# Performance work log

Measured on AMD Instinct MI355X. Metric: run time of the kernel, lower is better.

## Reference

```python
import jax, jax.numpy as jnp
import numpy as np

N = 50000      # nodes
E = 800000     # edges
F = 128        # feat_dim
N_RBF = 20
CUTOFF = 5.0


def setup_inputs() -> dict:
    key = jax.random.key(0)
    ks = jax.random.split(key, 10)
    s_j = jax.random.normal(ks[0], (N, F), dtype=jnp.float32)
    v_j = jax.random.normal(ks[1], (N, F, 3), dtype=jnp.float32)
    r_ij = jax.random.normal(ks[2], (E, 3), dtype=jnp.float32)
    nbrs = jax.random.randint(ks[3], (E, 2), 0, N, dtype=jnp.int64)
    # inv_dense: Dense(F->F, swish) then Dense(F->2F)
    W1 = jax.random.normal(ks[4], (F, F), dtype=jnp.float32) / np.sqrt(F)
    b1 = jnp.zeros((F,), dtype=jnp.float32)
    W2 = jax.random.normal(ks[5], (F, 2 * F), dtype=jnp.float32) / np.sqrt(F)
    b2 = jnp.zeros((2 * F,), dtype=jnp.float32)
    # dist_embed: PainnRadialBasis(n_rbf) -> Dense(n_rbf -> 2F), cosine envelope
    Wd = jax.random.normal(ks[6], (N_RBF, 2 * F), dtype=jnp.float32) / np.sqrt(N_RBF)
    bd = jnp.zeros((2 * F,), dtype=jnp.float32)
    return {"s_j": s_j, "v_j": v_j, "r_ij": r_ij, "nbrs": nbrs,
            "W1": W1, "b1": b1, "W2": W2, "b2": b2, "Wd": Wd, "bd": bd}


def reference(s_j, v_j, r_ij, nbrs, W1, b1, W2, b2, Wd, bd):
    # preprocess_r
    dist = jnp.sqrt(jnp.sum(r_ij ** 2 + 1e-8, axis=-1))        # [E]
    unit = r_ij / dist[:, None]                                 # [E,3]

    # InvariantMessage: per-node MLP then gather sender features
    h = jax.nn.silu(s_j @ W1 + b1)                              # [N,F]
    phi_all = h @ W2 + b2                                       # [N,2F]
    phi = phi_all[nbrs[:, 1]]                                   # [E,2F]

    # DistanceEmbed: PaiNN radial basis sin(n*pi*d/cutoff)/d -> Dense -> cosine envelope
    n = jnp.arange(1, N_RBF + 1, dtype=dist.dtype)              # [n_rbf]
    rbf = jnp.sin(n[None, :] * jnp.pi * dist[:, None] / CUTOFF) / dist[:, None]  # [E,n_rbf]
    w_s = rbf @ Wd + bd                                         # [E,2F]
    env = jnp.where(dist < CUTOFF, 0.5 * (jnp.cos(jnp.pi * dist / CUTOFF) + 1.0), 0.0)
    w_s = w_s * env[:, None]

    inv_out = (phi * w_s).reshape(E, 2, F)                      # [E,2,F]
    equi_filter = inv_out[:, 0, :][:, :, None]                  # [E,F,1]
    inv_filter = inv_out[:, 1, :]                               # [E,F]

    delta_v_ij = equi_filter * unit[:, None, :]                 # [E,F,3]
    dest = nbrs[:, 0]
    delta_v_i = jax.ops.segment_sum(delta_v_ij, dest, num_segments=N)  # [N,F,3]
    delta_s_i = jax.ops.segment_sum(inv_filter, dest, num_segments=N)  # [N,F]
    return delta_s_i, delta_v_i
```

## Files before the change

### kernel.cpp

```cpp
#include <hip/hip_runtime.h>
#include <hip/hip_bf16.h>
#include <cstdint>
#include <cstddef>

#define N_NODES 50000
#define N_EDGES 800000
#define FDIM    128
#define NRBF    20
#define CUTOFF_R 5.0f
#define PI_F 3.14159265358979323846f

__global__ void detect_kernel(const int* __restrict__ n32, int* __restrict__ flag)
{
    __shared__ int any;
    if (threadIdx.x == 0) any = 0;
    __syncthreads();
    int nz = 0;
    for (int k = threadIdx.x; k < 1024; k += 256)
        nz |= (n32[2 * k + 1] != 0) ? 1 : 0;
    if (nz) atomicOr(&any, 1);
    __syncthreads();
    if (threadIdx.x == 0) flag[0] = any ? 0 : 1;
}

__global__ __launch_bounds__(256) void node_mlp_kernel(
    const float* __restrict__ S,  const float* __restrict__ W1, const float* __restrict__ b1,
    const float* __restrict__ W2, const float* __restrict__ b2, float* __restrict__ PHI)
{
    __shared__ float sS[64][129];
    __shared__ float sW[2048];

    const int tid  = threadIdx.x;
    const int row0 = blockIdx.x * 64;

    for (int i = tid; i < 2048; i += 256) {
        int r  = i >> 5;
        int c4 = (i & 31) * 4;
        int gr = row0 + r; if (gr >= N_NODES) gr = N_NODES - 1;
        const float4 v = *reinterpret_cast<const float4*>(&S[(size_t)gr * FDIM + c4]);
        sS[r][c4 + 0] = v.x; sS[r][c4 + 1] = v.y; sS[r][c4 + 2] = v.z; sS[r][c4 + 3] = v.w;
    }

    const int ty = tid >> 4;
    const int tx = tid & 15;

    float acc1[4][8];
    #pragma unroll
    for (int i = 0; i < 4; ++i)
        #pragma unroll
        for (int j = 0; j < 8; ++j) acc1[i][j] = 0.f;

    for (int kk = 0; kk < 128; kk += 16) {
        __syncthreads();
        for (int i = tid; i < 512; i += 256) {
            int r = i >> 5; int c4 = (i & 31) * 4;
            const float4 v = *reinterpret_cast<const float4*>(&W1[(size_t)(kk + r) * 128 + c4]);
            sW[r * 128 + c4 + 0] = v.x; sW[r * 128 + c4 + 1] = v.y;
            sW[r * 128 + c4 + 2] = v.z; sW[r * 128 + c4 + 3] = v.w;
        }
        __syncthreads();
        #pragma unroll
        for (int k2 = 0; k2 < 16; ++k2) {
            float a[4], b[8];
            #pragma unroll
            for (int i = 0; i < 4; ++i) a[i] = sS[ty * 4 + i][kk + k2];
            #pragma unroll
            for (int j = 0; j < 8; ++j) b[j] = sW[k2 * 128 + tx + 16 * j];
            #pragma unroll
            for (int i = 0; i < 4; ++i)
                #pragma unroll
                for (int j = 0; j < 8; ++j) acc1[i][j] = fmaf(a[i], b[j], acc1[i][j]);
        }
    }
    #pragma unroll
    for (int i = 0; i < 4; ++i) {
        #pragma unroll
        for (int j = 0; j < 8; ++j) {
            const int c = tx + 16 * j;
            const float x = acc1[i][j] + b1[c];
            sS[ty * 4 + i][c] = x / (1.f + __expf(-x));
        }
    }

    float acc2[4][16];
    #pragma unroll
    for (int i = 0; i < 4; ++i)
        #pragma unroll
        for (int j = 0; j < 16; ++j) acc2[i][j] = 0.f;

    for (int kk = 0; kk < 128; kk += 8) {
        __syncthreads();
        for (int i = tid; i < 512; i += 256) {
            int r = i >> 6; int c4 = (i & 63) * 4;
            const float4 v = *reinterpret_cast<const float4*>(&W2[(size_t)(kk + r) * 256 + c4]);
            sW[r * 256 + c4 + 0] = v.x; sW[r * 256 + c4 + 1] = v.y;
            sW[r * 256 + c4 + 2] = v.z; sW[r * 256 + c4 + 3] = v.w;
        }
        __syncthreads();
        #pragma unroll
        for (int k2 = 0; k2 < 8; ++k2) {
            float a[4], b[16];
            #pragma unroll
            for (int i = 0; i < 4; ++i) a[i] = sS[ty * 4 + i][kk + k2];
            #pragma unroll
            for (int j = 0; j < 16; ++j) b[j] = sW[k2 * 256 + tx + 16 * j];
            #pragma unroll
            for (int i = 0; i < 4; ++i)
                #pragma unroll
                for (int j = 0; j < 16; ++j) acc2[i][j] = fmaf(a[i], b[j], acc2[i][j]);
        }
    }
    #pragma unroll
    for (int i = 0; i < 4; ++i) {
        const int gr = row0 + ty * 4 + i;
        if (gr < N_NODES) {
            #pragma unroll
            for (int j = 0; j < 16; ++j) {
                const int c = tx + 16 * j;
                PHI[(size_t)gr * 256 + c] = acc2[i][j] + b2[c];
            }
        }
    }
}

__global__ void hist_kernel(const int* __restrict__ n32, const int* __restrict__ flag,
                            int* __restrict__ counts)
{
    const int e = blockIdx.x * blockDim.x + threadIdx.x;
    const int str = flag[0] ? 4 : 2;
    if (e < N_EDGES) {
        const int d = n32[(size_t)str * e];
        atomicAdd(&counts[d], 1);
    }
}

__global__ __launch_bounds__(1024) void scan_kernel(const int* __restrict__ counts,
                                                    int* __restrict__ offsets,
                                                    int* __restrict__ cursor)
{
    __shared__ int sums[1024];
    const int t   = threadIdx.x;
    const int per = (N_NODES + 1023) / 1024;
    const int lo  = t * per;
    const int hi  = (lo + per < N_NODES) ? lo + per : N_NODES;
    int s = 0;
    for (int i = lo; i < hi; ++i) s += counts[i];
    sums[t] = s;
    __syncthreads();
    if (t == 0) {
        int run = 0;
        for (int i = 0; i < 1024; ++i) { const int v = sums[i]; sums[i] = run; run += v; }
        offsets[N_NODES] = run;
    }
    __syncthreads();
    int run = sums[t];
    for (int i = lo; i < hi; ++i) {
        offsets[i] = run;
        cursor[i]  = run;
        run += counts[i];
    }
}

__global__ void scatter_kernel(const int* __restrict__ n32, const int* __restrict__ flag,
                               int* __restrict__ cursor, int* __restrict__ csr)
{
    const int e = blockIdx.x * blockDim.x + threadIdx.x;
    const int str = flag[0] ? 4 : 2;
    if (e < N_EDGES) {
        const int d   = n32[(size_t)str * e];
        const int pos = atomicAdd(&cursor[d], 1);
        csr[pos] = e;
    }
}

__global__ __launch_bounds__(256, 3) void gather_kernel(
    const float* __restrict__ PHI, const float* __restrict__ r_ij,
    const int* __restrict__ n32, const int* __restrict__ flag,
    const float* __restrict__ Wd, const float* __restrict__ bd,
    const int* __restrict__ offsets, const int* __restrict__ csr,
    float* __restrict__ out_s, float* __restrict__ out_v)
{
    const int tid  = threadIdx.x;
    const int node = blockIdx.x * 4 + (tid >> 6);
    const int l    = tid & 63;
    if (node >= N_NODES) return;

    float wd[NRBF][4];
    #pragma unroll
    for (int n = 0; n < NRBF; ++n) {
        wd[n][0] = Wd[n * 256 + l      ];
        wd[n][1] = Wd[n * 256 + l + 64 ];
        wd[n][2] = Wd[n * 256 + l + 128];
        wd[n][3] = Wd[n * 256 + l + 192];
    }
    const float bd0 = bd[l], bd1 = bd[l + 64], bd2 = bd[l + 128], bd3 = bd[l + 192];

    const int f64  = flag[0];
    const int str  = f64 ? 4 : 2;
    const int soff = f64 ? 2 : 1;

    const int beg = offsets[node];
    const int end = offsets[node + 1];

    float as0 = 0.f, as1 = 0.f;
    float av0x = 0.f, av0y = 0.f, av0z = 0.f;
    float av1x = 0.f, av1y = 0.f, av1z = 0.f;

    if (beg < end) {
        int e = __builtin_amdgcn_readfirstlane(csr[beg]);
        int j = __builtin_amdgcn_readfirstlane(n32[(size_t)str * e + soff]);
        const float* ph = PHI + (size_t)j * 256;
        float p0 = ph[l], p1 = ph[l + 64], p2 = ph[l + 128], p3 = ph[l + 192];
        float rx = r_ij[3 * (size_t)e + 0];
        float ry = r_ij[3 * (size_t)e + 1];
        float rz = r_ij[3 * (size_t)e + 2];

        for (int p = beg; p < end; ++p) {
            const int pn = (p + 1 < end) ? (p + 1) : p;
            const int e2 = __builtin_amdgcn_readfirstlane(csr[pn]);
            const int j2 = __builtin_amdgcn_readfirstlane(n32[(size_t)str * e2 + soff]);
            const float* ph2 = PHI + (size_t)j2 * 256;
            const float q0 = ph2[l], q1 = ph2[l + 64], q2 = ph2[l + 128], q3 = ph2[l + 192];
            const float sx = r_ij[3 * (size_t)e2 + 0];
            const float sy = r_ij[3 * (size_t)e2 + 1];
            const float sz = r_ij[3 * (size_t)e2 + 2];

            const float d2    = fmaf(rx, rx, fmaf(ry, ry, fmaf(rz, rz, 3e-8f)));
            const float inv_d = __frsqrt_rn(d2);
            const float dist  = d2 * inv_d;
            const float x  = (PI_F / CUTOFF_R) * dist;
            const float sn = __sinf(x);
            const float cn = __cosf(x);
            const float env  = (dist < CUTOFF_R) ? (0.5f * (cn + 1.0f)) : 0.0f;
            const float twoc = cn + cn;

            float w0 = bd0, w1 = bd1, w2 = bd2, w3 = bd3;
            float sm1 = 0.f, scur = sn;
            #pragma unroll
            for (int n = 0; n < NRBF; ++n) {
                const float rb = scur * inv_d;
                w0 = fmaf(rb, wd[n][0], w0);
                w1 = fmaf(rb, wd[n][1], w1);
                w2 = fmaf(rb, wd[n][2], w2);
                w3 = fmaf(rb, wd[n][3], w3);
                const float nxt = fmaf(twoc, scur, -sm1);
                sm1 = scur; scur = nxt;
            }

            const float ux = rx * inv_d, uy = ry * inv_d, uz = rz * inv_d;
            const float e0 = p0 * (w0 * env);
            const float e1 = p1 * (w1 * env);
            as0 = fmaf(p2, w2 * env, as0);
            as1 = fmaf(p3, w3 * env, as1);
            av0x = fmaf(e0, ux, av0x); av0y = fmaf(e0, uy, av0y); av0z = fmaf(e0, uz, av0z);
            av1x = fmaf(e1, ux, av1x); av1y = fmaf(e1, uy, av1y); av1z = fmaf(e1, uz, av1z);

            p0 = q0; p1 = q1; p2 = q2; p3 = q3;
            rx = sx; ry = sy; rz = sz;
        }
    }

    out_s[(size_t)node * FDIM + l]      = as0;
    out_s[(size_t)node * FDIM + 64 + l] = as1;
    const size_t vb0 = ((size_t)node * FDIM + l) * 3;
    const size_t vb1 = ((size_t)node * FDIM + 64 + l) * 3;
    out_v[vb0 + 0] = av0x; out_v[vb0 + 1] = av0y; out_v[vb0 + 2] = av0z;
    out_v[vb1 + 0] = av1x; out_v[vb1 + 1] = av1y; out_v[vb1 + 2] = av1z;
}

extern "C" void kernel_launch(void* const* d_in, const int* in_sizes, int n_in,
                              void* d_out, int out_size, void* d_ws, size_t ws_size,
                              hipStream_t stream)
{
    (void)in_sizes; (void)n_in; (void)out_size; (void)ws_size;
    const float* s_j  = (const float*)d_in[0];
    const float* r_ij = (const float*)d_in[2];
    const int*   n32  = (const int*)d_in[3];
    const float* W1   = (const float*)d_in[4];
    const float* b1   = (const float*)d_in[5];
    const float* W2   = (const float*)d_in[6];
    const float* b2   = (const float*)d_in[7];
    const float* Wd   = (const float*)d_in[8];
    const float* bd   = (const float*)d_in[9];

    float* out_s = (float*)d_out;
    float* out_v = out_s + (size_t)N_NODES * FDIM;

    char*  ws      = (char*)d_ws;
    float* PHI     = (float*)(ws);
    int*   counts  = (int*)(ws + 51200000);
    int*   offsets = (int*)(ws + 51400000);
    int*   cursor  = (int*)(ws + 51600128);
    int*   csr     = (int*)(ws + 51800128);
    int*   flag    = (int*)(ws + 55000128);

    hipMemsetAsync(counts, 0, N_NODES * sizeof(int), stream);

    detect_kernel <<<1, 256, 0, stream>>>(n32, flag);
    node_mlp_kernel<<<(N_NODES + 63) / 64, 256, 0, stream>>>(s_j, W1, b1, W2, b2, PHI);
    hist_kernel   <<<(N_EDGES + 255) / 256, 256, 0, stream>>>(n32, flag, counts);
    scan_kernel   <<<1, 1024, 0, stream>>>(counts, offsets, cursor);
    scatter_kernel<<<(N_EDGES + 255) / 256, 256, 0, stream>>>(n32, flag, cursor, csr);
    gather_kernel <<<(N_NODES + 3) / 4, 256, 0, stream>>>(PHI, r_ij, n32, flag, Wd, bd,
                                                          offsets, csr, out_s, out_v);
}
```

Baseline: 715.0 us.

## Vectorize node MLP smem access, warp-shuffle scan, pin gather Wd registers

The node MLP switches to float4 shared-memory loads and stores, larger K tiles (32 and 16) and a padded row stride, which cuts LDS instructions and barriers. The scan kernel replaces its serial 1024-element pass with a wavefront shuffle scan plus a 16-entry serial pass. The gather kernel drops the occupancy hint of 3 blocks per CU from launch_bounds and uses an empty asm barrier to keep the Wd coefficients resident in VGPRs. In exchange the MLP changes its column-to-thread mapping, and the gather kernel may use more registers, which can lower occupancy.

```diff
diff --git a/kernel.cpp b/kernel.cpp
--- a/kernel.cpp
+++ b/kernel.cpp
@@ -27,87 +27,96 @@
     const float* __restrict__ S,  const float* __restrict__ W1, const float* __restrict__ b1,
     const float* __restrict__ W2, const float* __restrict__ b2, float* __restrict__ PHI)
 {
-    __shared__ float sS[64][129];
-    __shared__ float sW[2048];
+    __shared__ float sS[64][132];
+    __shared__ float sW[4096];
 
     const int tid  = threadIdx.x;
     const int row0 = blockIdx.x * 64;
+    const int ty   = tid >> 4;
+    const int tx   = tid & 15;
 
     for (int i = tid; i < 2048; i += 256) {
-        int r  = i >> 5;
-        int c4 = (i & 31) * 4;
+        const int r  = i >> 5;
+        const int c4 = (i & 31) * 4;
         int gr = row0 + r; if (gr >= N_NODES) gr = N_NODES - 1;
-        const float4 v = *reinterpret_cast<const float4*>(&S[(size_t)gr * FDIM + c4]);
-        sS[r][c4 + 0] = v.x; sS[r][c4 + 1] = v.y; sS[r][c4 + 2] = v.z; sS[r][c4 + 3] = v.w;
-    }
-
-    const int ty = tid >> 4;
-    const int tx = tid & 15;
+        *reinterpret_cast<float4*>(&sS[r][c4]) =
+            *reinterpret_cast<const float4*>(&S[(size_t)gr * FDIM + c4]);
+    }
 
     float acc1[4][8];
     #pragma unroll
     for (int i = 0; i < 4; ++i)
         #pragma unroll
         for (int j = 0; j < 8; ++j) acc1[i][j] = 0.f;
+
+    for (int kk = 0; kk < 128; kk += 32) {
+        __syncthreads();
+        for (int i = tid; i < 1024; i += 256) {
+            const int r  = i >> 5;
+            const int c4 = (i & 31) * 4;
+            *reinterpret_cast<float4*>(&sW[r * 128 + c4]) =
+                *reinterpret_cast<const float4*>(&W1[(size_t)(kk + r) * 128 + c4]);
+        }
+        __syncthreads();
+        #pragma unroll
+        for (int k2 = 0; k2 < 32; ++k2) {
+            float a[4];
+            #pragma unroll
+            for (int i = 0; i < 4; ++i) a[i] = sS[ty * 4 + i][kk + k2];
+            const float4 b0 = *reinterpret_cast<const float4*>(&sW[k2 * 128 + tx * 4]);
+            const float4 b4 = *reinterpret_cast<const float4*>(&sW[k2 * 128 + 64 + tx * 4]);
+            const float bb[8] = {b0.x, b0.y, b0.z, b0.w, b4.x, b4.y, b4.z, b4.w};
+            #pragma unroll
+            for (int i = 0; i < 4; ++i)
+                #pragma unroll
+                for (int j = 0; j < 8; ++j) acc1[i][j] = fmaf(a[i], bb[j], acc1[i][j]);
+        }
+    }
+    {
+        const float4 c0 = *reinterpret_cast<const float4*>(&b1[tx * 4]);
+        const float4 c4 = *reinterpret_cast<const float4*>(&b1[64 + tx * 4]);
+        const float bb[8] = {c0.x, c0.y, c0.z, c0.w, c4.x, c4.y, c4.z, c4.w};
+        #pragma unroll
+        for (int i = 0; i < 4; ++i) {
+            #pragma unroll
+            for (int j = 0; j < 8; ++j) {
+                const int c = (j < 4) ? (tx * 4 + j) : (64 + tx * 4 + (j - 4));
+                const float x = acc1[i][j] + bb[j];
+                sS[ty * 4 + i][c] = x / (1.f + __expf(-x));
+            }
+        }
+    }
+
+    float acc2[4][16];
+    #pragma unroll
+    for (int i = 0; i < 4; ++i)
+        #pragma unroll
+        for (int j = 0; j < 16; ++j) acc2[i][j] = 0.f;
 
     for (int kk = 0; kk < 128; kk += 16) {
         __syncthreads();
-        for (int i = tid; i < 512; i += 256) {
-            int r = i >> 5; int c4 = (i & 31) * 4;
-            const float4 v = *reinterpret_cast<const float4*>(&W1[(size_t)(kk + r) * 128 + c4]);
-            sW[r * 128 + c4 + 0] = v.x; sW[r * 128 + c4 + 1] = v.y;
-            sW[r * 128 + c4 + 2] = v.z; sW[r * 128 + c4 + 3] = v.w;
+        for (int i = tid; i < 1024; i += 256) {
+            const int r  = i >> 6;
+            const int c4 = (i & 63) * 4;
+            *reinterpret_cast<float4*>(&sW[r * 256 + c4]) =
+                *reinterpret_cast<const float4*>(&W2[(size_t)(kk + r) * 256 + c4]);
         }
         __syncthreads();
         #pragma unroll
         for (int k2 = 0; k2 < 16; ++k2) {
-            float a[4], b[8];
+            float a[4];
             #pragma unroll
             for (int i = 0; i < 4; ++i) a[i] = sS[ty * 4 + i][kk + k2];
             #pragma unroll
-            for (int j = 0; j < 8; ++j) b[j] = sW[k2 * 128 + tx + 16 * j];
-            #pragma unroll
-            for (int i = 0; i < 4; ++i)
+            for (int h = 0; h < 4; ++h) {
+                const float4 b = *reinterpret_cast<const float4*>(&sW[k2 * 256 + h * 64 + tx * 4]);
+                const float bb[4] = {b.x, b.y, b.z, b.w};
                 #pragma unroll
-                for (int j = 0; j < 8; ++j) acc1[i][j] = fmaf(a[i], b[j], acc1[i][j]);
-        }
-    }
-    #pragma unroll
-    for (int i = 0; i < 4; ++i) {
-        #pragma unroll
-        for (int j = 0; j < 8; ++j) {
-            const int c = tx + 16 * j;
-            const float x = acc1[i][j] + b1[c];
-            sS[ty * 4 + i][c] = x / (1.f + __expf(-x));
-        }
-    }
-
-    float acc2[4][16];
-    #pragma unroll
-    for (int i = 0; i < 4; ++i)
-        #pragma unroll
-        for (int j = 0; j < 16; ++j) acc2[i][j] = 0.f;
-
-    for (int kk = 0; kk < 128; kk += 8) {
-        __syncthreads();
-        for (int i = tid; i < 512; i += 256) {
-            int r = i >> 6; int c4 = (i & 63) * 4;
-            const float4 v = *reinterpret_cast<const float4*>(&W2[(size_t)(kk + r) * 256 + c4]);
-            sW[r * 256 + c4 + 0] = v.x; sW[r * 256 + c4 + 1] = v.y;
-            sW[r * 256 + c4 + 2] = v.z; sW[r * 256 + c4 + 3] = v.w;
-        }
-        __syncthreads();
-        #pragma unroll
-        for (int k2 = 0; k2 < 8; ++k2) {
-            float a[4], b[16];
-            #pragma unroll
-            for (int i = 0; i < 4; ++i) a[i] = sS[ty * 4 + i][kk + k2];
-            #pragma unroll
-            for (int j = 0; j < 16; ++j) b[j] = sW[k2 * 256 + tx + 16 * j];
-            #pragma unroll
-            for (int i = 0; i < 4; ++i)
-                #pragma unroll
-                for (int j = 0; j < 16; ++j) acc2[i][j] = fmaf(a[i], b[j], acc2[i][j]);
+                for (int i = 0; i < 4; ++i)
+                    #pragma unroll
+                    for (int j = 0; j < 4; ++j)
+                        acc2[i][h * 4 + j] = fmaf(a[i], bb[j], acc2[i][h * 4 + j]);
+            }
         }
     }
     #pragma unroll
@@ -115,9 +124,14 @@
         const int gr = row0 + ty * 4 + i;
         if (gr < N_NODES) {
             #pragma unroll
-            for (int j = 0; j < 16; ++j) {
-                const int c = tx + 16 * j;
-                PHI[(size_t)gr * 256 + c] = acc2[i][j] + b2[c];
+            for (int h = 0; h < 4; ++h) {
+                const float4 c = *reinterpret_cast<const float4*>(&b2[h * 64 + tx * 4]);
+                float4 o;
+                o.x = acc2[i][h * 4 + 0] + c.x;
+                o.y = acc2[i][h * 4 + 1] + c.y;
+                o.z = acc2[i][h * 4 + 2] + c.z;
+                o.w = acc2[i][h * 4 + 3] + c.w;
+                *reinterpret_cast<float4*>(&PHI[(size_t)gr * 256 + h * 64 + tx * 4]) = o;
             }
         }
     }
@@ -138,22 +152,34 @@
                                                     int* __restrict__ offsets,
                                                     int* __restrict__ cursor)
 {
-    __shared__ int sums[1024];
-    const int t   = threadIdx.x;
-    const int per = (N_NODES + 1023) / 1024;
-    const int lo  = t * per;
-    const int hi  = (lo + per < N_NODES) ? lo + per : N_NODES;
+    __shared__ int wsum[16];
+    const int t    = threadIdx.x;
+    const int lane = t & 63;
+    const int wid  = t >> 6;
+    const int per  = (N_NODES + 1023) / 1024;
+    const int lo   = t * per;
+    const int hi   = (lo + per < N_NODES) ? lo + per : N_NODES;
+
     int s = 0;
     for (int i = lo; i < hi; ++i) s += counts[i];
-    sums[t] = s;
+
+    int inc = s;
+    #pragma unroll
+    for (int off = 1; off < 64; off <<= 1) {
+        const int v = __shfl_up(inc, off, 64);
+        if (lane >= off) inc += v;
+    }
+    if (lane == 63) wsum[wid] = inc;
     __syncthreads();
     if (t == 0) {
         int run = 0;
-        for (int i = 0; i < 1024; ++i) { const int v = sums[i]; sums[i] = run; run += v; }
+        #pragma unroll
+        for (int i = 0; i < 16; ++i) { const int v = wsum[i]; wsum[i] = run; run += v; }
         offsets[N_NODES] = run;
     }
     __syncthreads();
-    int run = sums[t];
+
+    int run = wsum[wid] + inc - s;
     for (int i = lo; i < hi; ++i) {
         offsets[i] = run;
         cursor[i]  = run;
@@ -173,7 +199,7 @@
     }
 }
 
-__global__ __launch_bounds__(256, 3) void gather_kernel(
+__global__ __launch_bounds__(256) void gather_kernel(
     const float* __restrict__ PHI, const float* __restrict__ r_ij,
     const int* __restrict__ n32, const int* __restrict__ flag,
     const float* __restrict__ Wd, const float* __restrict__ bd,
@@ -185,13 +211,17 @@
     const int l    = tid & 63;
     if (node >= N_NODES) return;
 
-    float wd[NRBF][4];
+    float wd0[NRBF], wd1[NRBF], wd2[NRBF], wd3[NRBF];
     #pragma unroll
     for (int n = 0; n < NRBF; ++n) {
-        wd[n][0] = Wd[n * 256 + l      ];
-        wd[n][1] = Wd[n * 256 + l + 64 ];
-        wd[n][2] = Wd[n * 256 + l + 128];
-        wd[n][3] = Wd[n * 256 + l + 192];
+        wd0[n] = Wd[n * 256 + l      ];
+        wd1[n] = Wd[n * 256 + l + 64 ];
+        wd2[n] = Wd[n * 256 + l + 128];
+        wd3[n] = Wd[n * 256 + l + 192];
+    }
+    #pragma unroll
+    for (int n = 0; n < NRBF; ++n) {
+        asm volatile("" : "+v"(wd0[n]), "+v"(wd1[n]), "+v"(wd2[n]), "+v"(wd3[n]));
     }
     const float bd0 = bd[l], bd1 = bd[l + 64], bd2 = bd[l + 128], bd3 = bd[l + 192];
 
@@ -239,10 +269,10 @@
             #pragma unroll
             for (int n = 0; n < NRBF; ++n) {
                 const float rb = scur * inv_d;
-                w0 = fmaf(rb, wd[n][0], w0);
-                w1 = fmaf(rb, wd[n][1], w1);
-                w2 = fmaf(rb, wd[n][2], w2);
-                w3 = fmaf(rb, wd[n][3], w3);
+                w0 = fmaf(rb, wd0[n], w0);
+                w1 = fmaf(rb, wd1[n], w1);
+                w2 = fmaf(rb, wd2[n], w2);
+                w3 = fmaf(rb, wd3[n], w3);
                 const float nxt = fmaf(twoc, scur, -sm1);
                 sm1 = scur; scur = nxt;
             }
```

Measured after the change: 676.5 us. -5.4%, faster.
